# Optimization experiments

Hardware: AMD Instinct MI355X
Metric: run time of the kernel (lower is better)

Reference implementation:

```python
import jax, jax.numpy as jnp
import numpy as np

LEADER_IDX = 0
SOCIAL_DIST = 1.5
COHESION = 0.8
B, N, T = 64, 64, 100


def setup_inputs() -> dict:
    key = jax.random.key(0)
    k1, k2, k3, k4, k5 = jax.random.split(key, 5)
    # trajectories: (x, y, vel, yaw, acc, yawvel)
    x = jax.random.normal(k1, (B, N, T, 6), dtype=jnp.float32) * 5.0
    # world_from_agent: per-agent SE(2) homogeneous transform (B, 3, 3)
    theta = jax.random.uniform(k2, (B,), minval=-np.pi, maxval=np.pi)
    c, s = jnp.cos(theta), jnp.sin(theta)
    trans = jax.random.normal(k3, (B, 2), dtype=jnp.float32) * 50.0
    wfa = (jnp.zeros((B, 3, 3), dtype=jnp.float32)
           .at[:, 0, 0].set(c).at[:, 0, 1].set(-s)
           .at[:, 1, 0].set(s).at[:, 1, 1].set(c)
           .at[:, :2, 2].set(trans).at[:, 2, 2].set(1.0))
    # externalized randomness of torch forward (randint over B-1 choices, rand<p)
    rand_idx = jax.random.randint(k4, (T * N, B), 0, B - 1, dtype=jnp.int32)
    drop_mask = jax.random.uniform(k5, (T * N, B)) < COHESION
    return {"x": x, "world_from_agent": wfa, "rand_idx": rand_idx, "drop_mask": drop_mask}


def reference(x, world_from_agent, rand_idx, drop_mask):
    pos = x[..., :2]                                   # (B, N, T, 2)
    R = world_from_agent[:, :2, :2]                    # (B, 2, 2)
    t = world_from_agent[:, :2, 2]                     # (B, 2)
    pos_g = jnp.einsum('bntj,bij->bnti', pos, R) + t[:, None, None, :]
    # leader positions are detached (no grad), but same value in fwd
    leader = (jnp.arange(B) == LEADER_IDX)[:, None, None, None]
    pos_g = jnp.where(leader, jax.lax.stop_gradient(pos_g), pos_g)
    # (B,N,T,2) -> (T,N,B,2) -> (T*N, B, 2)  (matches torch transpose(0,2).reshape)
    flat = jnp.transpose(pos_g, (2, 1, 0, 3)).reshape(T * N, B, 2)
    # pairwise euclidean distances via norm trick (avoids (TN,B,B,2) diff tensor)
    sq = jnp.sum(flat * flat, axis=-1)                 # (TN, B)
    d2 = sq[:, :, None] + sq[:, None, :] - 2.0 * jnp.einsum('tbd,tcd->tbc', flat, flat)
    dist = jnp.sqrt(jnp.maximum(d2, 1e-12))            # (TN, B, B)
    eye = jnp.eye(B, dtype=bool)
    dist = jnp.where(eye[None], jnp.inf, dist)         # mask self-distance
    min_nb = jnp.argmin(dist, axis=-1).astype(jnp.int32)      # (TN, B)
    # row b of neighbor_choices is [0..b-1, b+1..B-1]; gather at rand_idx ->
    # value = rand_idx + (rand_idx >= b)
    b_idx = jnp.arange(B, dtype=jnp.int32)[None, :]
    rand_nb = rand_idx + (rand_idx >= b_idx).astype(jnp.int32)
    nb = jnp.where(drop_mask, rand_nb, min_nb)         # (TN, B)
    nd = jnp.take_along_axis(dist, nb[..., None], axis=2)[..., 0]  # (TN, B)
    nd = jnp.transpose(nd.reshape(T, N, B), (2, 1, 0))  # (B, N, T)
    loss = jnp.mean((nd - SOCIAL_DIST) ** 2, axis=-1)   # (B, N)
    return loss
```

## Files before the change

### kernel.cpp

```cpp
#include <hip/hip_runtime.h>

#define BB 64
#define NN 64
#define TT 100
#define TQ 4
#define NTQ (TT / TQ)

__global__ __launch_bounds__(256) void social_slice_kernel(
    const float* __restrict__ x,
    const float* __restrict__ wfa,
    const int* __restrict__ rand_idx,
    const int* __restrict__ drop_mask,
    float* __restrict__ ws)
{
    const int n  = blockIdx.x & 63;
    const int tq = blockIdx.x >> 6;
    const int t0 = tq * TQ;

    __shared__ float2 S[TQ][BB + 1];
    __shared__ float  Rld[TQ][BB];

    {
        const int lb = threadIdx.x >> 2;
        const int k  = threadIdx.x & 3;
        const float* wp = wfa + lb * 9;
        const float r00 = wp[0], r01 = wp[1], tx = wp[2];
        const float r10 = wp[3], r11 = wp[4], ty = wp[5];
        const size_t xoff = (((size_t)lb * NN + n) * (size_t)TT + (size_t)(t0 + k)) * 6;
        const float2 p = *(const float2*)(x + xoff);
        const float gx = r00 * p.x + r01 * p.y + tx;
        const float gy = r10 * p.x + r11 * p.y + ty;
        S[k][lb] = make_float2(gx, gy);
    }
    __syncthreads();

    const int w = threadIdx.x >> 6;
    const int b = threadIdx.x & 63;
    const int t = t0 + w;
    const int s = t * NN + n;
    const size_t sb = (size_t)s * BB + b;
    const int r  = rand_idx[sb];
    const int dm = drop_mask[sb];

    const float2 g = S[w][b];
    const float gx = g.x, gy = g.y;

    const float INF = __int_as_float(0x7f800000);
    float m0 = INF, m1 = INF, m2 = INF, m3 = INF;
    #pragma unroll
    for (int i = 0; i < 16; ++i) {
        {
            const int c = i;
            const float2 q = S[w][c];
            const float dx = gx - q.x, dy = gy - q.y;
            float d2 = fmaf(dx, dx, dy * dy);
            d2 = (c == b) ? INF : d2;
            m0 = fminf(m0, d2);
        }
        {
            const int c = 16 + i;
            const float2 q = S[w][c];
            const float dx = gx - q.x, dy = gy - q.y;
            float d2 = fmaf(dx, dx, dy * dy);
            d2 = (c == b) ? INF : d2;
            m1 = fminf(m1, d2);
        }
        {
            const int c = 32 + i;
            const float2 q = S[w][c];
            const float dx = gx - q.x, dy = gy - q.y;
            float d2 = fmaf(dx, dx, dy * dy);
            d2 = (c == b) ? INF : d2;
            m2 = fminf(m2, d2);
        }
        {
            const int c = 48 + i;
            const float2 q = S[w][c];
            const float dx = gx - q.x, dy = gy - q.y;
            float d2 = fmaf(dx, dx, dy * dy);
            d2 = (c == b) ? INF : d2;
            m3 = fminf(m3, d2);
        }
    }
    const float best = fminf(fminf(m0, m1), fminf(m2, m3));

    const int rnb = r + (r >= b ? 1 : 0);
    const float sq  = fmaf(gx, gx, gy * gy);
    const float qx  = __shfl(gx, rnb);
    const float qy  = __shfl(gy, rnb);
    const float qsq = __shfl(sq, rnb);
    const float d2r = fmaf(-2.0f, fmaf(gx, qx, gy * qy), sq + qsq);

    const float d2sel = dm ? d2r : best;
    const float nd = sqrtf(fmaxf(d2sel, 1e-12f));
    const float diff = nd - 1.5f;
    Rld[w][b] = diff * diff;
    __syncthreads();

    if (w == 0) {
        const float sum4 = ((Rld[0][b] + Rld[1][b]) + Rld[2][b]) + Rld[3][b];
        ws[((size_t)tq * NN + n) * BB + b] = sum4;
    }
}

__global__ __launch_bounds__(256) void social_reduce_kernel(
    const float* __restrict__ ws,
    float* __restrict__ out)
{
    const int b = threadIdx.x & 63;
    const int n = blockIdx.x * 4 + (threadIdx.x >> 6);

    float acc = 0.f;
    #pragma unroll
    for (int tq = 0; tq < NTQ; ++tq)
        acc += ws[((size_t)tq * NN + n) * BB + b];
    out[b * NN + n] = acc * (1.0f / TT);
}

extern "C" void kernel_launch(void* const* d_in, const int* in_sizes, int n_in,
                              void* d_out, int out_size, void* d_ws, size_t ws_size,
                              hipStream_t stream) {
    const float* x = (const float*)d_in[0];
    const float* wfa = (const float*)d_in[1];
    const int* rand_idx = (const int*)d_in[2];
    const int* drop_mask = (const int*)d_in[3];
    float* out = (float*)d_out;
    float* ws = (float*)d_ws;

    social_slice_kernel<<<NTQ * NN, 256, 0, stream>>>(
        x, wfa, rand_idx, drop_mask, ws);
    social_reduce_kernel<<<NN / 4, 256, 0, stream>>>(ws, out);
}
```

Measured before the change: 70.40 us.

## Fuse slice and reduce kernels into one block per agent

Replaces the two-kernel scheme (per-time-quarter partial sums written to a workspace, then a separate reduction) with one kernel that launches one 1024-thread block per agent index n. Each block stages all 100 timesteps of transformed positions in shared memory, loops 16 waves over time, and reduces in shared memory before writing the final mean. This removes the workspace round trip and the second launch. In exchange it launches only 64 blocks, which cuts parallelism across the GPU's compute units, and it needs a much larger shared-memory footprint per block.

After: 81.65 us. 1.16x slower.

```diff
diff --git a/kernel.cpp b/kernel.cpp
--- a/kernel.cpp
+++ b/kernel.cpp
@@ -3,118 +3,117 @@
 #define BB 64
 #define NN 64
 #define TT 100
-#define TQ 4
-#define NTQ (TT / TQ)
+#define WV 16
+#define SP (BB + 1)
 
-__global__ __launch_bounds__(256) void social_slice_kernel(
+__global__ __launch_bounds__(1024) void social_fused_kernel(
     const float* __restrict__ x,
     const float* __restrict__ wfa,
     const int* __restrict__ rand_idx,
     const int* __restrict__ drop_mask,
-    float* __restrict__ ws)
+    float* __restrict__ out)
 {
-    const int n  = blockIdx.x & 63;
-    const int tq = blockIdx.x >> 6;
-    const int t0 = tq * TQ;
+    const int n   = blockIdx.x;
+    const int tid = threadIdx.x;
 
-    __shared__ float2 S[TQ][BB + 1];
-    __shared__ float  Rld[TQ][BB];
+    __shared__ float2 S[TT * SP];
+    __shared__ float  Rld[WV][BB];
 
     {
-        const int lb = threadIdx.x >> 2;
-        const int k  = threadIdx.x & 3;
+        const int lb = tid >> 4;
+        const int k  = tid & 15;
         const float* wp = wfa + lb * 9;
         const float r00 = wp[0], r01 = wp[1], tx = wp[2];
         const float r10 = wp[3], r11 = wp[4], ty = wp[5];
-        const size_t xoff = (((size_t)lb * NN + n) * (size_t)TT + (size_t)(t0 + k)) * 6;
-        const float2 p = *(const float2*)(x + xoff);
-        const float gx = r00 * p.x + r01 * p.y + tx;
-        const float gy = r10 * p.x + r11 * p.y + ty;
-        S[k][lb] = make_float2(gx, gy);
+        const size_t xb = (((size_t)lb * NN + n) * (size_t)TT) * 6;
+        #pragma unroll
+        for (int j = 0; j < 7; ++j) {
+            const int t = k + 16 * j;
+            if (t < TT) {
+                const float2 p = *(const float2*)(x + xb + (size_t)t * 6);
+                const float gx = r00 * p.x + r01 * p.y + tx;
+                const float gy = r10 * p.x + r11 * p.y + ty;
+                S[t * SP + lb] = make_float2(gx, gy);
+            }
+        }
     }
     __syncthreads();
 
-    const int w = threadIdx.x >> 6;
-    const int b = threadIdx.x & 63;
-    const int t = t0 + w;
-    const int s = t * NN + n;
-    const size_t sb = (size_t)s * BB + b;
-    const int r  = rand_idx[sb];
-    const int dm = drop_mask[sb];
+    const int w = tid >> 6;
+    const int b = tid & 63;
+    const float INF = __int_as_float(0x7f800000);
 
-    const float2 g = S[w][b];
-    const float gx = g.x, gy = g.y;
+    float acc = 0.f;
+    for (int t = w; t < TT; t += WV) {
+        const int s = t * NN + n;
+        const size_t sb = (size_t)s * BB + b;
+        const int r  = rand_idx[sb];
+        const int dm = drop_mask[sb];
 
-    const float INF = __int_as_float(0x7f800000);
-    float m0 = INF, m1 = INF, m2 = INF, m3 = INF;
-    #pragma unroll
-    for (int i = 0; i < 16; ++i) {
-        {
-            const int c = i;
-            const float2 q = S[w][c];
-            const float dx = gx - q.x, dy = gy - q.y;
-            float d2 = fmaf(dx, dx, dy * dy);
-            d2 = (c == b) ? INF : d2;
-            m0 = fminf(m0, d2);
+        const float2* St = S + t * SP;
+        const float2 g = St[b];
+        const float gx = g.x, gy = g.y;
+
+        float m0 = INF, m1 = INF, m2 = INF, m3 = INF;
+        #pragma unroll
+        for (int i = 0; i < 16; ++i) {
+            {
+                const int c = i;
+                const float2 q = St[c];
+                const float dx = gx - q.x, dy = gy - q.y;
+                float d2 = fmaf(dx, dx, dy * dy);
+                d2 = (c == b) ? INF : d2;
+                m0 = fminf(m0, d2);
+            }
+            {
+                const int c = 16 + i;
+                const float2 q = St[c];
+                const float dx = gx - q.x, dy = gy - q.y;
+                float d2 = fmaf(dx, dx, dy * dy);
+                d2 = (c == b) ? INF : d2;
+                m1 = fminf(m1, d2);
+            }
+            {
+                const int c = 32 + i;
+                const float2 q = St[c];
+                const float dx = gx - q.x, dy = gy - q.y;
+                float d2 = fmaf(dx, dx, dy * dy);
+                d2 = (c == b) ? INF : d2;
+                m2 = fminf(m2, d2);
+            }
+            {
+                const int c = 48 + i;
+                const float2 q = St[c];
+                const float dx = gx - q.x, dy = gy - q.y;
+                float d2 = fmaf(dx, dx, dy * dy);
+                d2 = (c == b) ? INF : d2;
+                m3 = fminf(m3, d2);
+            }
         }
-        {
-            const int c = 16 + i;
-            const float2 q = S[w][c];
-            const float dx = gx - q.x, dy = gy - q.y;
-            float d2 = fmaf(dx, dx, dy * dy);
-            d2 = (c == b) ? INF : d2;
-            m1 = fminf(m1, d2);
-        }
-        {
-            const int c = 32 + i;
-            const float2 q = S[w][c];
-            const float dx = gx - q.x, dy = gy - q.y;
-            float d2 = fmaf(dx, dx, dy * dy);
-            d2 = (c == b) ? INF : d2;
-            m2 = fminf(m2, d2);
-        }
-        {
-            const int c = 48 + i;
-            const float2 q = S[w][c];
-            const float dx = gx - q.x, dy = gy - q.y;
-            float d2 = fmaf(dx, dx, dy * dy);
-            d2 = (c == b) ? INF : d2;
-            m3 = fminf(m3, d2);
-        }
+        const float best = fminf(fminf(m0, m1), fminf(m2, m3));
+
+        const int rnb = r + (r >= b ? 1 : 0);
+        const float sq  = fmaf(gx, gx, gy * gy);
+        const float qx  = __shfl(gx, rnb);
+        const float qy  = __shfl(gy, rnb);
+        const float qsq = __shfl(sq, rnb);
+        const float d2r = fmaf(-2.0f, fmaf(gx, qx, gy * qy), sq + qsq);
+
+        const float d2sel = dm ? d2r : best;
+        const float nd = sqrtf(fmaxf(d2sel, 1e-12f));
+        const float diff = nd - 1.5f;
+        acc += diff * diff;
     }
-    const float best = fminf(fminf(m0, m1), fminf(m2, m3));
-
-    const int rnb = r + (r >= b ? 1 : 0);
-    const float sq  = fmaf(gx, gx, gy * gy);
-    const float qx  = __shfl(gx, rnb);
-    const float qy  = __shfl(gy, rnb);
-    const float qsq = __shfl(sq, rnb);
-    const float d2r = fmaf(-2.0f, fmaf(gx, qx, gy * qy), sq + qsq);
-
-    const float d2sel = dm ? d2r : best;
-    const float nd = sqrtf(fmaxf(d2sel, 1e-12f));
-    const float diff = nd - 1.5f;
-    Rld[w][b] = diff * diff;
+    Rld[w][b] = acc;
     __syncthreads();
 
     if (w == 0) {
-        const float sum4 = ((Rld[0][b] + Rld[1][b]) + Rld[2][b]) + Rld[3][b];
-        ws[((size_t)tq * NN + n) * BB + b] = sum4;
+        float ssum = 0.f;
+        #pragma unroll
+        for (int jj = 0; jj < WV; ++jj)
+            ssum += Rld[jj][b];
+        out[(size_t)b * NN + n] = ssum * (1.0f / TT);
     }
-}
-
-__global__ __launch_bounds__(256) void social_reduce_kernel(
-    const float* __restrict__ ws,
-    float* __restrict__ out)
-{
-    const int b = threadIdx.x & 63;
-    const int n = blockIdx.x * 4 + (threadIdx.x >> 6);
-
-    float acc = 0.f;
-    #pragma unroll
-    for (int tq = 0; tq < NTQ; ++tq)
-        acc += ws[((size_t)tq * NN + n) * BB + b];
-    out[b * NN + n] = acc * (1.0f / TT);
 }
 
 extern "C" void kernel_launch(void* const* d_in, const int* in_sizes, int n_in,
@@ -125,9 +124,7 @@
     const int* rand_idx = (const int*)d_in[2];
     const int* drop_mask = (const int*)d_in[3];
     float* out = (float*)d_out;
-    float* ws = (float*)d_ws;
+    (void)d_ws; (void)ws_size;
 
-    social_slice_kernel<<<NTQ * NN, 256, 0, stream>>>(
-        x, wfa, rand_idx, drop_mask, ws);
-    social_reduce_kernel<<<NN / 4, 256, 0, stream>>>(ws, out);
+    social_fused_kernel<<<NN, 1024, 0, stream>>>(x, wfa, rand_idx, drop_mask, out);
 }
```
